# Optimization experiments

Measured on AMD Instinct MI355X. Metric: run time of the kernel, lower is better.

Reference implementation:

```python
import jax, jax.numpy as jnp
import numpy as np

HEADS = 16

def setup_inputs() -> dict:
    key = jax.random.key(0)
    ks = jax.random.split(key, 5)
    dim = 1024
    x = jax.random.normal(ks[0], (2, 2048, dim), dtype=jnp.float32)
    scale = 1.0 / np.sqrt(dim)
    Wq = jax.random.normal(ks[1], (dim, dim), dtype=jnp.float32) * scale
    Wk = jax.random.normal(ks[2], (dim, dim), dtype=jnp.float32) * scale
    Wv = jax.random.normal(ks[3], (dim, dim), dtype=jnp.float32) * scale
    Wo = jax.random.normal(ks[4], (dim, dim), dtype=jnp.float32) * scale
    return {"x": x, "Wq": Wq, "Wk": Wk, "Wv": Wv, "Wo": Wo}

def reference(x, Wq, Wk, Wv, Wo):
    b, n, dim = x.shape
    h = HEADS
    d = dim // h
    # projections: torch Linear y = x @ W.T (W is [out,in])
    def split_heads(t):
        return t.reshape(b, n, h, d).transpose(0, 2, 1, 3)  # b h n d
    q = split_heads(x @ Wq.T)
    k = split_heads(x @ Wk.T)
    v = split_heads(x @ Wv.T)
    scale = jnp.asarray(d, x.dtype) ** -0.5
    dots = jnp.einsum('bhid,bhjd->bhij', q, k) * scale
    # causal mask: positions j > i masked (triu with diagonal 1 since i == j)
    i_idx = jnp.arange(n)[:, None]
    j_idx = jnp.arange(n)[None, :]
    mask_value = -jnp.finfo(dots.dtype).max
    dots = jnp.where(j_idx > i_idx, mask_value, dots)
    attn = jax.nn.softmax(dots, axis=-1)  # dropout p=0 (eval) is identity
    out = jnp.einsum('bhij,bhjd->bhid', attn, v)
    out = out.transpose(0, 2, 1, 3).reshape(b, n, dim)
    return out @ Wo.T
```

## Files before the change

### kernel.cpp

```cpp
#include <hip/hip_runtime.h>
#include <hip/hip_bf16.h>

#define BATCH 2
#define SEQ   2048
#define DIM   1024
#define HEADS 16
#define DIMH  64
#define LOG2E 1.44269504088896340736f
#define SM_SHIFT 16.0f

typedef __attribute__((ext_vector_type(8))) short short8;
typedef __attribute__((ext_vector_type(4))) short short4v;
typedef __attribute__((ext_vector_type(4))) float floatx4;

#if defined(__has_builtin)
#if __has_builtin(__builtin_amdgcn_mfma_f32_16x16x16bf16_1k)
#define HAVE_MFMA16 1
#endif
#endif

static __device__ __forceinline__ void gload_lds16(const void* g, void* l) {
    __builtin_amdgcn_global_load_lds(
        (const __attribute__((address_space(1))) void*)g,
        (__attribute__((address_space(3))) void*)l, 16, 0, 0);
}

static __device__ __forceinline__ unsigned pk_trunc(float a, float b) {
    return (__float_as_uint(b) & 0xffff0000u) | (__float_as_uint(a) >> 16);
}

__global__ __launch_bounds__(256) void conv_all(
    const float* __restrict__ x,  const float* __restrict__ Wq,
    const float* __restrict__ Wk, const float* __restrict__ Wv,
    const float* __restrict__ Wo,
    __hip_bfloat16* __restrict__ dst, __hip_bfloat16* __restrict__ dwo)
{
    const size_t NX = (size_t)BATCH * SEQ * DIM;
    const size_t NW = (size_t)DIM * DIM;
    size_t i = ((size_t)blockIdx.x * 256 + threadIdx.x) * 4;
    if (i >= NX + 4 * NW) return;
    const float* src; __hip_bfloat16* d;
    if (i < NX) { src = x + i; d = dst + i; }
    else if (i < NX + 3 * NW) {
        size_t j = i - NX;
        int w = (int)(j >> 20);
        src = ((w == 0) ? Wq : (w == 1) ? Wk : Wv) + (j & (NW - 1));
        d = dst + i;
    } else {
        size_t off = i - (NX + 3 * NW);
        src = Wo + off; d = dwo + off;
    }
    floatx4 f = *reinterpret_cast<const floatx4*>(src);
    short4v o;
    #pragma unroll
    for (int e = 0; e < 4; ++e) {
        __hip_bfloat16 t = __float2bfloat16(f[e]);
        o[e] = *reinterpret_cast<short*>(&t);
    }
    *reinterpret_cast<short4v*>(d) = o;
}

__global__ __launch_bounds__(256) void gemm_qkv(
    const __hip_bfloat16* __restrict__ xbf,
    const __hip_bfloat16* __restrict__ wbf,
    __hip_bfloat16* __restrict__ qkv)
{
    __shared__ __align__(16) short As[128 * 64];
    __shared__ __align__(16) short Bs[128 * 64];

    const int tid  = threadIdx.x;
    const int wv   = tid >> 6;
    const int lane = tid & 63;
    const int quad = lane >> 4;
    const int l16  = lane & 15;
    const int xr   = l16 & 7;
    const int wm   = wv >> 1, wn = wv & 1;
    const int m0   = blockIdx.x * 128;
    const int n0   = blockIdx.y * 128;
    const int z    = n0 >> 10;
    __hip_bfloat16* out = qkv + (size_t)z * (BATCH * SEQ * DIM);

    const int srow = tid >> 3;
    const int sjc  = tid & 7;

    floatx4 acc[4][4] = {};

    for (int k0 = 0; k0 < DIM; k0 += 64) {
        __syncthreads();
        #pragma unroll
        for (int i = 0; i < 4; ++i) {
            const int row = srow + i * 32;
            const int sg  = sjc ^ (row & 7);
            gload_lds16(xbf + (size_t)(m0 + row) * DIM + k0 + sg * 8,
                        (char*)As + i * 4096 + wv * 1024);
            gload_lds16(wbf + (size_t)(n0 + row) * DIM + k0 + sg * 8,
                        (char*)Bs + i * 4096 + wv * 1024);
        }
        __syncthreads();

        short8 af[2][4], bf_[2][4];
        #pragma unroll
        for (int kk = 0; kk < 2; ++kk) {
            #pragma unroll
            for (int mt = 0; mt < 4; ++mt)
                af[kk][mt] = *reinterpret_cast<const short8*>(
                    &As[(wm * 64 + mt * 16 + l16) * 64 + ((kk * 4 + quad) ^ xr) * 8]);
            #pragma unroll
            for (int nt = 0; nt < 4; ++nt)
                bf_[kk][nt] = *reinterpret_cast<const short8*>(
                    &Bs[(wn * 64 + nt * 16 + l16) * 64 + ((kk * 4 + quad) ^ xr) * 8]);
        }
        #pragma unroll
        for (int kk = 0; kk < 2; ++kk)
            #pragma unroll
            for (int mt = 0; mt < 4; ++mt)
                #pragma unroll
                for (int nt = 0; nt < 4; ++nt)
                    acc[mt][nt] = __builtin_amdgcn_mfma_f32_16x16x32_bf16(
                        af[kk][mt], bf_[kk][nt], acc[mt][nt], 0, 0, 0);
    }

    const float esc = (z == 0) ? (0.125f * LOG2E) : 1.0f;
    #pragma unroll
    for (int mt = 0; mt < 4; ++mt) {
        #pragma unroll
        for (int nt = 0; nt < 4; ++nt) {
            const int n  = n0 + wn * 64 + nt * 16 + l16;
            const int hh = (n >> 6) & 15, dv = n & 63;
            #pragma unroll
            for (int r = 0; r < 4; ++r) {
                const int m  = m0 + wm * 64 + mt * 16 + quad * 4 + r;
                const int bb = m >> 11, nn = m & (SEQ - 1);
                const float v = acc[mt][nt][r] * esc;
                if (z < 2)
                    out[((size_t)(bb * HEADS + hh) * SEQ + nn) * DIMH + dv] = __float2bfloat16(v);
                else
                    out[((size_t)(bb * HEADS + hh) * DIMH + dv) * SEQ + nn] = __float2bfloat16(v);
            }
        }
    }
}

__global__ __launch_bounds__(256) void gemm_out(
    const __hip_bfloat16* __restrict__ qhs,
    const __hip_bfloat16* __restrict__ W,
    float* __restrict__ C)
{
    __shared__ __align__(16) short As[64 * 64];
    __shared__ __align__(16) short Bs[128 * 64];

    const int tid  = threadIdx.x;
    const int wv   = tid >> 6;
    const int lane = tid & 63;
    const int quad = lane >> 4;
    const int l16  = lane & 15;
    const int xr   = l16 & 7;
    const int wm   = wv >> 1, wn = wv & 1;
    const int m0   = blockIdx.x * 64;
    const int n0   = blockIdx.y * 128;

    const int srow = tid >> 3;
    const int sjc  = tid & 7;

    floatx4 acc[2][4] = {};

    for (int k0 = 0; k0 < DIM; k0 += 64) {
        const int h = k0 >> 6;
        __syncthreads();
        #pragma unroll
        for (int i = 0; i < 2; ++i) {
            const int row = srow + i * 32;
            const int sg  = sjc ^ (row & 7);
            const int m   = m0 + row;
            const int bb  = m >> 11, nn = m & (SEQ - 1);
            gload_lds16(qhs + ((size_t)(bb * HEADS + h) * SEQ + nn) * DIMH + sg * 8,
                        (char*)As + i * 4096 + wv * 1024);
        }
        #pragma unroll
        for (int i = 0; i < 4; ++i) {
            const int row = srow + i * 32;
            const int sg  = sjc ^ (row & 7);
            gload_lds16(W + (size_t)(n0 + row) * DIM + k0 + sg * 8,
                        (char*)Bs + i * 4096 + wv * 1024);
        }
        __syncthreads();

        short8 af[2][2], bf_[2][4];
        #pragma unroll
        for (int kk = 0; kk < 2; ++kk) {
            #pragma unroll
            for (int mt = 0; mt < 2; ++mt)
                af[kk][mt] = *reinterpret_cast<const short8*>(
                    &As[(wm * 32 + mt * 16 + l16) * 64 + ((kk * 4 + quad) ^ xr) * 8]);
            #pragma unroll
            for (int nt = 0; nt < 4; ++nt)
                bf_[kk][nt] = *reinterpret_cast<const short8*>(
                    &Bs[(wn * 64 + nt * 16 + l16) * 64 + ((kk * 4 + quad) ^ xr) * 8]);
        }
        #pragma unroll
        for (int kk = 0; kk < 2; ++kk)
            #pragma unroll
            for (int mt = 0; mt < 2; ++mt)
                #pragma unroll
                for (int nt = 0; nt < 4; ++nt)
                    acc[mt][nt] = __builtin_amdgcn_mfma_f32_16x16x32_bf16(
                        af[kk][mt], bf_[kk][nt], acc[mt][nt], 0, 0, 0);
    }

    #pragma unroll
    for (int mt = 0; mt < 2; ++mt)
        #pragma unroll
        for (int nt = 0; nt < 4; ++nt) {
            const int n = n0 + wn * 64 + nt * 16 + l16;
            #pragma unroll
            for (int r = 0; r < 4; ++r) {
                const int m = m0 + wm * 32 + mt * 16 + quad * 4 + r;
                C[(size_t)m * DIM + n] = acc[mt][nt][r];
            }
        }
}

__global__ __launch_bounds__(128) void attn_causal(
    __hip_bfloat16* __restrict__ qkv)
{
    __shared__ __align__(16) short kt[64 * 64];
    __shared__ __align__(16) short vt[64 * 64];
#if !defined(HAVE_MFMA16)
    __shared__ __align__(16) short pt[2][16 * 72];
#endif

    const int id    = blockIdx.x;
    const int combo = id & 31;
    const int p     = id >> 5;
    const int b     = combo >> 4;
    const int h     = combo & 15;
    const int tA = p, tB = 63 - p;
    const int nA = (tA + 2) >> 1;
    const int nB = (tB + 2) >> 1;
    const int total = nA + nB;

    const size_t hoff = (size_t)(b * HEADS + h) * SEQ * DIMH;
    const size_t one  = (size_t)BATCH * SEQ * DIM;
    __hip_bfloat16* qb        = qkv + hoff;
    const __hip_bfloat16* kb  = qkv + one + hoff;
    const __hip_bfloat16* vtg = qkv + 2 * one + hoff;

    const int tid  = threadIdx.x;
    const int wv   = tid >> 6;
    const int lane = tid & 63;
    const int quad = lane >> 4;
    const int l16  = lane & 15;
    const int xr   = l16 & 7;

    int q16 = tA * 32 + wv * 16;
    short8 aq0 = *reinterpret_cast<const short8*>(qb + (size_t)(q16 + l16) * DIMH + quad * 8);
    short8 aq1 = *reinterpret_cast<const short8*>(qb + (size_t)(q16 + l16) * DIMH + 32 + quad * 8);
    floatx4 oacc[4] = {};
    floatx4 lsum = {};

    const int srow = tid >> 3;
    const int sch  = (tid & 7) ^ (srow & 7);

#if defined(HAVE_MFMA16)
    const short4v kone4 = {0x3F80, 0x3F80, 0x3F80, 0x3F80};
#else
    const short8 kone8 = {0x3F80, 0x3F80, 0x3F80, 0x3F80,
                          0x3F80, 0x3F80, 0x3F80, 0x3F80};
#endif

    short8 kreg[4], vreg[4];
    #pragma unroll
    for (int i = 0; i < 4; ++i) {
        const int c = tid + 128 * i;
        const int row = c >> 3, jc = c & 7;
        kreg[i] = *reinterpret_cast<const short8*>(kb + (size_t)row * DIMH + jc * 8);
        vreg[i] = *reinterpret_cast<const short8*>(vtg + (size_t)row * SEQ + jc * 8);
    }

    for (int s = 0; s < total; ++s) {
        const bool lastA = (s == nA - 1);
        const int j0 = ((s < nA) ? s : s - nA) * 64;

        __syncthreads();
        #pragma unroll
        for (int i = 0; i < 4; ++i) {
            const int c = tid + 128 * i;
            const int row = c >> 3, jc = c & 7;
            const int off = row * 64 + ((jc ^ (row & 7)) * 8);
            *reinterpret_cast<short8*>(&kt[off]) = kreg[i];
            *reinterpret_cast<short8*>(&vt[off]) = vreg[i];
        }
        __syncthreads();

        if (s + 1 < total) {
            const int s2 = s + 1;
            const int j1 = ((s2 < nA) ? s2 : s2 - nA) * 64;
            #pragma unroll
            for (int i = 0; i < 4; ++i) {
                const int c = tid + 128 * i;
                const int row = c >> 3, jc = c & 7;
                kreg[i] = *reinterpret_cast<const short8*>(kb + (size_t)(j1 + row) * DIMH + jc * 8);
                vreg[i] = *reinterpret_cast<const short8*>(vtg + (size_t)row * SEQ + j1 + jc * 8);
            }
        }

        floatx4 st[4];
        #pragma unroll
        for (int t = 0; t < 4; ++t) {
            const int rw = t * 16 + l16;
            short8 a0 = *reinterpret_cast<const short8*>(&kt[rw * 64 + (quad ^ xr) * 8]);
            short8 a1 = *reinterpret_cast<const short8*>(&kt[rw * 64 + ((quad + 4) ^ xr) * 8]);
            floatx4 zz = {};
            zz    = __builtin_amdgcn_mfma_f32_16x16x32_bf16(a0, aq0, zz, 0, 0, 0);
            st[t] = __builtin_amdgcn_mfma_f32_16x16x32_bf16(a1, aq1, zz, 0, 0, 0);
        }

        if (j0 + 63 > q16) {
            const int qg = q16 + l16;
            #pragma unroll
            for (int t = 0; t < 4; ++t)
                #pragma unroll
                for (int r = 0; r < 4; ++r) {
                    const int jg = j0 + t * 16 + quad * 4 + r;
                    if (jg > qg) st[t][r] = -3.0e38f;
                }
        }

        #pragma unroll
        for (int t = 0; t < 4; ++t)
            #pragma unroll
            for (int r = 0; r < 4; ++r)
                st[t][r] = __builtin_amdgcn_exp2f(st[t][r] - SM_SHIFT);

#if defined(HAVE_MFMA16)
        short4v pa[4];
        #pragma unroll
        for (int t = 0; t < 4; ++t) {
            unsigned u2[2] = { pk_trunc(st[t][0], st[t][1]),
                               pk_trunc(st[t][2], st[t][3]) };
            pa[t] = *reinterpret_cast<short4v*>(u2);
        }
        #pragma unroll
        for (int t = 0; t < 4; ++t)
            lsum = __builtin_amdgcn_mfma_f32_16x16x16bf16_1k(pa[t], kone4, lsum, 0, 0, 0);
        #pragma unroll
        for (int dt = 0; dt < 4; ++dt) {
            const int row = dt * 16 + l16;
            #pragma unroll
            for (int t = 0; t < 4; ++t) {
                short4v bv = *reinterpret_cast<const short4v*>(
                    &vt[row * 64 + (((t * 2 + (quad >> 1)) ^ xr) * 8) + (quad & 1) * 4]);
                oacc[dt] = __builtin_amdgcn_mfma_f32_16x16x16bf16_1k(pa[t], bv, oacc[dt], 0, 0, 0);
            }
        }
        if (lastA || s == total - 1) {
            #pragma unroll
            for (int r = 0; r < 4; ++r) {
                const float rl = 1.0f / lsum[r];
                #pragma unroll
                for (int dt = 0; dt < 4; ++dt)
                    qb[(size_t)(q16 + quad * 4 + r) * DIMH + dt * 16 + l16] =
                        __float2bfloat16(oacc[dt][r] * rl);
            }
#else
        #pragma unroll
        for (int t = 0; t < 4; ++t) {
            *reinterpret_cast<unsigned*>(&pt[wv][l16 * 72 + t * 16 + quad * 4]) =
                pk_trunc(st[t][0], st[t][1]);
            *reinterpret_cast<unsigned*>(&pt[wv][l16 * 72 + t * 16 + quad * 4 + 2]) =
                pk_trunc(st[t][2], st[t][3]);
        }
        short8 p0 = *reinterpret_cast<const short8*>(&pt[wv][l16 * 72 + quad * 8]);
        short8 p1 = *reinterpret_cast<const short8*>(&pt[wv][l16 * 72 + 32 + quad * 8]);
        lsum = __builtin_amdgcn_mfma_f32_16x16x32_bf16(kone8, p0, lsum, 0, 0, 0);
        lsum = __builtin_amdgcn_mfma_f32_16x16x32_bf16(kone8, p1, lsum, 0, 0, 0);
        #pragma unroll
        for (int dt = 0; dt < 4; ++dt) {
            const int rw = dt * 16 + l16;
            short8 v0 = *reinterpret_cast<const short8*>(&vt[rw * 64 + (quad ^ xr) * 8]);
            short8 v1 = *reinterpret_cast<const short8*>(&vt[rw * 64 + ((quad + 4) ^ xr) * 8]);
            oacc[dt] = __builtin_amdgcn_mfma_f32_16x16x32_bf16(v0, p0, oacc[dt], 0, 0, 0);
            oacc[dt] = __builtin_amdgcn_mfma_f32_16x16x32_bf16(v1, p1, oacc[dt], 0, 0, 0);
        }
        if (lastA || s == total - 1) {
            const float rl = 1.0f / lsum[0];
            #pragma unroll
            for (int dt = 0; dt < 4; ++dt)
                #pragma unroll
                for (int r = 0; r < 4; ++r)
                    qb[(size_t)(q16 + l16) * DIMH + dt * 16 + quad * 4 + r] =
                        __float2bfloat16(oacc[dt][r] * rl);
#endif
            if (lastA) {
                q16 = tB * 32 + wv * 16;
                aq0 = *reinterpret_cast<const short8*>(qb + (size_t)(q16 + l16) * DIMH + quad * 8);
                aq1 = *reinterpret_cast<const short8*>(qb + (size_t)(q16 + l16) * DIMH + 32 + quad * 8);
                #pragma unroll
                for (int dt = 0; dt < 4; ++dt)
                    #pragma unroll
                    for (int r = 0; r < 4; ++r) oacc[dt][r] = 0.f;
                #pragma unroll
                for (int r = 0; r < 4; ++r) lsum[r] = 0.f;
            }
        }
    }
}


extern "C" void kernel_launch(void* const* d_in, const int* in_sizes, int n_in,
                              void* d_out, int out_size, void* d_ws, size_t ws_size,
                              hipStream_t stream) {
    const float* x  = (const float*)d_in[0];
    const float* Wq = (const float*)d_in[1];
    const float* Wk = (const float*)d_in[2];
    const float* Wv = (const float*)d_in[3];
    const float* Wo = (const float*)d_in[4];

    __hip_bfloat16* qkv  = (__hip_bfloat16*)d_ws;
    __hip_bfloat16* wobf = (__hip_bfloat16*)((char*)d_ws + (size_t)24 * 1024 * 1024);

    __hip_bfloat16* xbf = (__hip_bfloat16*)d_out;
    __hip_bfloat16* wbf = xbf + (size_t)BATCH * SEQ * DIM;

    conv_all  <<<8192, 256, 0, stream>>>(x, Wq, Wk, Wv, Wo, xbf, wobf);
    gemm_qkv  <<<dim3((BATCH * SEQ) / 128, (3 * DIM) / 128), 256, 0, stream>>>(xbf, wbf, qkv);
    attn_causal<<<dim3(1024), 128, 0, stream>>>(qkv);
    gemm_out  <<<dim3((BATCH * SEQ) / 64, DIM / 128), 256, 0, stream>>>(qkv, wobf, (float*)d_out);
}
```

Baseline: 201.5 us.

## Use single-wave attention blocks with register K/V fragments and larger output GEMM tiles

The attention kernel moves from 128-thread blocks sharing K/V tiles in LDS to 64-thread single-wave blocks that load K and V MFMA fragments straight from global memory into registers. This removes the block barriers and LDS staging, and launches twice as many blocks with 16-row query tiles. It also drops the 16x16x16 MFMA path in favor of the 32-wide path with a small LDS transpose for P. The output GEMM tile grows from 64x128 to 128x128 for more reuse per block. The trade-offs are more global K/V traffic, since waves no longer share tiles, and higher register pressure.

```diff
diff --git a/kernel.cpp b/kernel.cpp
--- a/kernel.cpp
+++ b/kernel.cpp
@@ -12,12 +12,6 @@
 typedef __attribute__((ext_vector_type(8))) short short8;
 typedef __attribute__((ext_vector_type(4))) short short4v;
 typedef __attribute__((ext_vector_type(4))) float floatx4;
-
-#if defined(__has_builtin)
-#if __has_builtin(__builtin_amdgcn_mfma_f32_16x16x16bf16_1k)
-#define HAVE_MFMA16 1
-#endif
-#endif
 
 static __device__ __forceinline__ void gload_lds16(const void* g, void* l) {
     __builtin_amdgcn_global_load_lds(
@@ -146,7 +140,7 @@
     const __hip_bfloat16* __restrict__ W,
     float* __restrict__ C)
 {
-    __shared__ __align__(16) short As[64 * 64];
+    __shared__ __align__(16) short As[128 * 64];
     __shared__ __align__(16) short Bs[128 * 64];
 
     const int tid  = threadIdx.x;
@@ -156,42 +150,37 @@
     const int l16  = lane & 15;
     const int xr   = l16 & 7;
     const int wm   = wv >> 1, wn = wv & 1;
-    const int m0   = blockIdx.x * 64;
+    const int m0   = blockIdx.x * 128;
     const int n0   = blockIdx.y * 128;
 
     const int srow = tid >> 3;
     const int sjc  = tid & 7;
 
-    floatx4 acc[2][4] = {};
+    floatx4 acc[4][4] = {};
 
     for (int k0 = 0; k0 < DIM; k0 += 64) {
         const int h = k0 >> 6;
         __syncthreads();
         #pragma unroll
-        for (int i = 0; i < 2; ++i) {
+        for (int i = 0; i < 4; ++i) {
             const int row = srow + i * 32;
             const int sg  = sjc ^ (row & 7);
             const int m   = m0 + row;
             const int bb  = m >> 11, nn = m & (SEQ - 1);
             gload_lds16(qhs + ((size_t)(bb * HEADS + h) * SEQ + nn) * DIMH + sg * 8,
                         (char*)As + i * 4096 + wv * 1024);
-        }
-        #pragma unroll
-        for (int i = 0; i < 4; ++i) {
-            const int row = srow + i * 32;
-            const int sg  = sjc ^ (row & 7);
             gload_lds16(W + (size_t)(n0 + row) * DIM + k0 + sg * 8,
                         (char*)Bs + i * 4096 + wv * 1024);
         }
         __syncthreads();
 
-        short8 af[2][2], bf_[2][4];
+        short8 af[2][4], bf_[2][4];
         #pragma unroll
         for (int kk = 0; kk < 2; ++kk) {
             #pragma unroll
-            for (int mt = 0; mt < 2; ++mt)
+            for (int mt = 0; mt < 4; ++mt)
                 af[kk][mt] = *reinterpret_cast<const short8*>(
-                    &As[(wm * 32 + mt * 16 + l16) * 64 + ((kk * 4 + quad) ^ xr) * 8]);
+                    &As[(wm * 64 + mt * 16 + l16) * 64 + ((kk * 4 + quad) ^ xr) * 8]);
             #pragma unroll
             for (int nt = 0; nt < 4; ++nt)
                 bf_[kk][nt] = *reinterpret_cast<const short8*>(
@@ -200,7 +189,7 @@
         #pragma unroll
         for (int kk = 0; kk < 2; ++kk)
             #pragma unroll
-            for (int mt = 0; mt < 2; ++mt)
+            for (int mt = 0; mt < 4; ++mt)
                 #pragma unroll
                 for (int nt = 0; nt < 4; ++nt)
                     acc[mt][nt] = __builtin_amdgcn_mfma_f32_16x16x32_bf16(
@@ -208,35 +197,31 @@
     }
 
     #pragma unroll
-    for (int mt = 0; mt < 2; ++mt)
+    for (int mt = 0; mt < 4; ++mt)
         #pragma unroll
         for (int nt = 0; nt < 4; ++nt) {
             const int n = n0 + wn * 64 + nt * 16 + l16;
             #pragma unroll
             for (int r = 0; r < 4; ++r) {
-                const int m = m0 + wm * 32 + mt * 16 + quad * 4 + r;
+                const int m = m0 + wm * 64 + mt * 16 + quad * 4 + r;
                 C[(size_t)m * DIM + n] = acc[mt][nt][r];
             }
         }
 }
 
-__global__ __launch_bounds__(128) void attn_causal(
+__global__ __launch_bounds__(64) void attn_causal(
     __hip_bfloat16* __restrict__ qkv)
 {
-    __shared__ __align__(16) short kt[64 * 64];
-    __shared__ __align__(16) short vt[64 * 64];
-#if !defined(HAVE_MFMA16)
-    __shared__ __align__(16) short pt[2][16 * 72];
-#endif
+    __shared__ __align__(16) short pt[16 * 72];
 
     const int id    = blockIdx.x;
     const int combo = id & 31;
     const int p     = id >> 5;
     const int b     = combo >> 4;
     const int h     = combo & 15;
-    const int tA = p, tB = 63 - p;
-    const int nA = (tA + 2) >> 1;
-    const int nB = (tB + 2) >> 1;
+    const int tA = p, tB = 127 - p;
+    const int nA = (tA >> 2) + 1;
+    const int nB = (tB >> 2) + 1;
     const int total = nA + nB;
 
     const size_t hoff = (size_t)(b * HEADS + h) * SEQ * DIMH;
@@ -245,74 +230,56 @@
     const __hip_bfloat16* kb  = qkv + one + hoff;
     const __hip_bfloat16* vtg = qkv + 2 * one + hoff;
 
-    const int tid  = threadIdx.x;
-    const int wv   = tid >> 6;
-    const int lane = tid & 63;
+    const int lane = threadIdx.x & 63;
     const int quad = lane >> 4;
     const int l16  = lane & 15;
-    const int xr   = l16 & 7;
-
-    int q16 = tA * 32 + wv * 16;
+
+    const short8 kone8 = {0x3F80, 0x3F80, 0x3F80, 0x3F80,
+                          0x3F80, 0x3F80, 0x3F80, 0x3F80};
+
+    int q16 = tA * 16;
     short8 aq0 = *reinterpret_cast<const short8*>(qb + (size_t)(q16 + l16) * DIMH + quad * 8);
     short8 aq1 = *reinterpret_cast<const short8*>(qb + (size_t)(q16 + l16) * DIMH + 32 + quad * 8);
     floatx4 oacc[4] = {};
     floatx4 lsum = {};
 
-    const int srow = tid >> 3;
-    const int sch  = (tid & 7) ^ (srow & 7);
-
-#if defined(HAVE_MFMA16)
-    const short4v kone4 = {0x3F80, 0x3F80, 0x3F80, 0x3F80};
-#else
-    const short8 kone8 = {0x3F80, 0x3F80, 0x3F80, 0x3F80,
-                          0x3F80, 0x3F80, 0x3F80, 0x3F80};
-#endif
-
-    short8 kreg[4], vreg[4];
+    short8 kf[4][2];
     #pragma unroll
-    for (int i = 0; i < 4; ++i) {
-        const int c = tid + 128 * i;
-        const int row = c >> 3, jc = c & 7;
-        kreg[i] = *reinterpret_cast<const short8*>(kb + (size_t)row * DIMH + jc * 8);
-        vreg[i] = *reinterpret_cast<const short8*>(vtg + (size_t)row * SEQ + jc * 8);
+    for (int t = 0; t < 4; ++t) {
+        const __hip_bfloat16* kr = kb + (size_t)(t * 16 + l16) * DIMH + quad * 8;
+        kf[t][0] = *reinterpret_cast<const short8*>(kr);
+        kf[t][1] = *reinterpret_cast<const short8*>(kr + 32);
     }
 
     for (int s = 0; s < total; ++s) {
         const bool lastA = (s == nA - 1);
         const int j0 = ((s < nA) ? s : s - nA) * 64;
 
-        __syncthreads();
-        #pragma unroll
-        for (int i = 0; i < 4; ++i) {
-            const int c = tid + 128 * i;
-            const int row = c >> 3, jc = c & 7;
-            const int off = row * 64 + ((jc ^ (row & 7)) * 8);
-            *reinterpret_cast<short8*>(&kt[off]) = kreg[i];
-            *reinterpret_cast<short8*>(&vt[off]) = vreg[i];
-        }
-        __syncthreads();
+        short8 vf[4][2];
+        #pragma unroll
+        for (int dt = 0; dt < 4; ++dt) {
+            const __hip_bfloat16* vr = vtg + (size_t)(dt * 16 + l16) * SEQ + j0 + quad * 8;
+            vf[dt][0] = *reinterpret_cast<const short8*>(vr);
+            vf[dt][1] = *reinterpret_cast<const short8*>(vr + 32);
+        }
+
+        floatx4 st[4];
+        #pragma unroll
+        for (int t = 0; t < 4; ++t) {
+            floatx4 zz = {};
+            zz    = __builtin_amdgcn_mfma_f32_16x16x32_bf16(kf[t][0], aq0, zz, 0, 0, 0);
+            st[t] = __builtin_amdgcn_mfma_f32_16x16x32_bf16(kf[t][1], aq1, zz, 0, 0, 0);
+        }
 
         if (s + 1 < total) {
             const int s2 = s + 1;
             const int j1 = ((s2 < nA) ? s2 : s2 - nA) * 64;
             #pragma unroll
-            for (int i = 0; i < 4; ++i) {
-                const int c = tid + 128 * i;
-                const int row = c >> 3, jc = c & 7;
-                kreg[i] = *reinterpret_cast<const short8*>(kb + (size_t)(j1 + row) * DIMH + jc * 8);
-                vreg[i] = *reinterpret_cast<const short8*>(vtg + (size_t)row * SEQ + j1 + jc * 8);
+            for (int t = 0; t < 4; ++t) {
+                const __hip_bfloat16* kr = kb + (size_t)(j1 + t * 16 + l16) * DIMH + quad * 8;
+                kf[t][0] = *reinterpret_cast<const short8*>(kr);
+                kf[t][1] = *reinterpret_cast<const short8*>(kr + 32);
             }
-        }
-
-        floatx4 st[4];
-        #pragma unroll
-        for (int t = 0; t < 4; ++t) {
-            const int rw = t * 16 + l16;
-            short8 a0 = *reinterpret_cast<const short8*>(&kt[rw * 64 + (quad ^ xr) * 8]);
-            short8 a1 = *reinterpret_cast<const short8*>(&kt[rw * 64 + ((quad + 4) ^ xr) * 8]);
-            floatx4 zz = {};
-            zz    = __builtin_amdgcn_mfma_f32_16x16x32_bf16(a0, aq0, zz, 0, 0, 0);
-            st[t] = __builtin_amdgcn_mfma_f32_16x16x32_bf16(a1, aq1, zz, 0, 0, 0);
         }
 
         if (j0 + 63 > q16) {
@@ -332,56 +299,25 @@
             for (int r = 0; r < 4; ++r)
                 st[t][r] = __builtin_amdgcn_exp2f(st[t][r] - SM_SHIFT);
 
-#if defined(HAVE_MFMA16)
-        short4v pa[4];
         #pragma unroll
         for (int t = 0; t < 4; ++t) {
-            unsigned u2[2] = { pk_trunc(st[t][0], st[t][1]),
-                               pk_trunc(st[t][2], st[t][3]) };
-            pa[t] = *reinterpret_cast<short4v*>(u2);
-        }
-        #pragma unroll
-        for (int t = 0; t < 4; ++t)
-            lsum = __builtin_amdgcn_mfma_f32_16x16x16bf16_1k(pa[t], kone4, lsum, 0, 0, 0);
-        #pragma unroll
-        for (int dt = 0; dt < 4; ++dt) {
-            const int row = dt * 16 + l16;
-            #pragma unroll
-            for (int t = 0; t < 4; ++t) {
-                short4v bv = *reinterpret_cast<const short4v*>(
-                    &vt[row * 64 + (((t * 2 + (quad >> 1)) ^ xr) * 8) + (quad & 1) * 4]);
-                oacc[dt] = __builtin_amdgcn_mfma_f32_16x16x16bf16_1k(pa[t], bv, oacc[dt], 0, 0, 0);
-            }
-        }
-        if (lastA || s == total - 1) {
-            #pragma unroll
-            for (int r = 0; r < 4; ++r) {
-                const float rl = 1.0f / lsum[r];
-                #pragma unroll
-                for (int dt = 0; dt < 4; ++dt)
-                    qb[(size_t)(q16 + quad * 4 + r) * DIMH + dt * 16 + l16] =
-                        __float2bfloat16(oacc[dt][r] * rl);
-            }
-#else
-        #pragma unroll
-        for (int t = 0; t < 4; ++t) {
-            *reinterpret_cast<unsigned*>(&pt[wv][l16 * 72 + t * 16 + quad * 4]) =
+            *reinterpret_cast<unsigned*>(&pt[l16 * 72 + t * 16 + quad * 4]) =
                 pk_trunc(st[t][0], st[t][1]);
-            *reinterpret_cast<unsigned*>(&pt[wv][l16 * 72 + t * 16 + quad * 4 + 2]) =
+            *reinterpret_cast<unsigned*>(&pt[l16 * 72 + t * 16 + quad * 4 + 2]) =
                 pk_trunc(st[t][2], st[t][3]);
         }
-        short8 p0 = *reinterpret_cast<const short8*>(&pt[wv][l16 * 72 + quad * 8]);
-        short8 p1 = *reinterpret_cast<const short8*>(&pt[wv][l16 * 72 + 32 + quad * 8]);
+        short8 p0 = *reinterpret_cast<const short8*>(&pt[l16 * 72 + quad * 8]);
+        short8 p1 = *reinterpret_cast<const short8*>(&pt[l16 * 72 + 32 + quad * 8]);
+
         lsum = __builtin_amdgcn_mfma_f32_16x16x32_bf16(kone8, p0, lsum, 0, 0, 0);
         lsum = __builtin_amdgcn_mfma_f32_16x16x32_bf16(kone8, p1, lsum, 0, 0, 0);
+
         #pragma unroll
         for (int dt = 0; dt < 4; ++dt) {
-            const int rw = dt * 16 + l16;
-            short8 v0 = *reinterpret_cast<const short8*>(&vt[rw * 64 + (quad ^ xr) * 8]);
-            short8 v1 = *reinterpret_cast<const short8*>(&vt[rw * 64 + ((quad + 4) ^ xr) * 8]);
-            oacc[dt] = __builtin_amdgcn_mfma_f32_16x16x32_bf16(v0, p0, oacc[dt], 0, 0, 0);
-            oacc[dt] = __builtin_amdgcn_mfma_f32_16x16x32_bf16(v1, p1, oacc[dt], 0, 0, 0);
-        }
+            oacc[dt] = __builtin_amdgcn_mfma_f32_16x16x32_bf16(vf[dt][0], p0, oacc[dt], 0, 0, 0);
+            oacc[dt] = __builtin_amdgcn_mfma_f32_16x16x32_bf16(vf[dt][1], p1, oacc[dt], 0, 0, 0);
+        }
+
         if (lastA || s == total - 1) {
             const float rl = 1.0f / lsum[0];
             #pragma unroll
@@ -390,9 +326,8 @@
                 for (int r = 0; r < 4; ++r)
                     qb[(size_t)(q16 + l16) * DIMH + dt * 16 + quad * 4 + r] =
                         __float2bfloat16(oacc[dt][r] * rl);
-#endif
             if (lastA) {
-                q16 = tB * 32 + wv * 16;
+                q16 = tB * 16;
                 aq0 = *reinterpret_cast<const short8*>(qb + (size_t)(q16 + l16) * DIMH + quad * 8);
                 aq1 = *reinterpret_cast<const short8*>(qb + (size_t)(q16 + l16) * DIMH + 32 + quad * 8);
                 #pragma unroll
@@ -424,6 +359,6 @@
 
     conv_all  <<<8192, 256, 0, stream>>>(x, Wq, Wk, Wv, Wo, xbf, wobf);
     gemm_qkv  <<<dim3((BATCH * SEQ) / 128, (3 * DIM) / 128), 256, 0, stream>>>(xbf, wbf, qkv);
-    attn_causal<<<dim3(1024), 128, 0, stream>>>(qkv);
-    gemm_out  <<<dim3((BATCH * SEQ) / 64, DIM / 128), 256, 0, stream>>>(qkv, wobf, (float*)d_out);
-}
+    attn_causal<<<dim3(2048), 64, 0, stream>>>(qkv);
+    gemm_out  <<<dim3((BATCH * SEQ) / 128, DIM / 128), 256, 0, stream>>>(qkv, wobf, (float*)d_out);
+}
```

Result: slower. 274.3 us (+36.1%).
